# Optimization experiments

Measured on AMD Instinct MI355X. Metric: run time of the kernel, lower is better.

The kernel has to match this reference:

```python
import jax, jax.numpy as jnp
import numpy as np

N = 100000
E = 1600000
D_IN, D_HID, D_OUT = 128, 128, 64
SLOPE = 0.01


def setup_inputs() -> dict:
    key = jax.random.key(0)
    k1, k2, k3, k4 = jax.random.split(key, 4)
    x = jax.random.normal(k1, (N, D_IN), dtype=jnp.float32)
    edge_index = jax.random.randint(k2, (2, E), 0, N, dtype=jnp.int64)
    W1 = jax.random.normal(k3, (D_HID, D_IN), dtype=jnp.float32) * 0.05
    b1 = jnp.zeros((D_HID,), dtype=jnp.float32)
    W2 = jax.random.normal(k4, (D_OUT, D_HID), dtype=jnp.float32) * 0.05
    b2 = jnp.zeros((D_OUT,), dtype=jnp.float32)
    return {"x": x, "edge_index": edge_index, "W1": W1, "b1": b1, "W2": W2, "b2": b2}


def _gcn_norm(edge_index, num_nodes):
    # PyG GCNConv: add self loops, symmetric normalization deg^{-1/2} A_hat deg^{-1/2}
    loops = jnp.arange(num_nodes, dtype=edge_index.dtype)
    src = jnp.concatenate([edge_index[0], loops])
    dst = jnp.concatenate([edge_index[1], loops])
    deg = jax.ops.segment_sum(jnp.ones_like(dst, dtype=jnp.float32), dst, num_segments=num_nodes)
    dinv = jnp.where(deg > 0, jax.lax.rsqrt(deg), 0.0)
    norm = dinv[src] * dinv[dst]  # [E+N]
    return src, dst, norm


def _gcn_conv(x, src, dst, norm, W, b):
    h = x @ W.T                              # [N, out]
    msg = h[src] * norm[:, None]             # gather + edge scale: [E+N, out]
    agg = jax.ops.segment_sum(msg, dst, num_segments=x.shape[0])  # scatter-add
    return agg + b


def reference(x, edge_index, W1, b1, W2, b2):
    src, dst, norm = _gcn_norm(edge_index, x.shape[0])
    h1 = jax.nn.leaky_relu(_gcn_conv(x, src, dst, norm, W1, b1), negative_slope=SLOPE)
    h2 = _gcn_conv(h1, src, dst, norm, W2, b2)  # logits, no activation on last layer
    return (h1, h2)
```

## Files before the change

kernel.cpp:

```cpp
#include <hip/hip_runtime.h>


#define THREADS 256

typedef __attribute__((ext_vector_type(8))) short bf16x8;
typedef __attribute__((ext_vector_type(4))) float f32x4;

__device__ __forceinline__ short f2bf_rne(float f) {
    unsigned u = __builtin_bit_cast(unsigned, f);
    u = u + 0x7fffu + ((u >> 16) & 1u);
    return (short)(u >> 16);
}
__device__ __forceinline__ float bf2f(short h) {
    unsigned u = ((unsigned)(unsigned short)h) << 16;
    return __builtin_bit_cast(float, u);
}

__global__ __launch_bounds__(THREADS)
void count_kernel(const int* __restrict__ dst, int* __restrict__ counts, int E, int T) {
    int t = blockIdx.x * THREADS + threadIdx.x;
    int e0 = t, e1 = t + T, e2 = t + 2 * T, e3 = t + 3 * T;
    int d0 = dst[e0], d1 = dst[e1], d2 = dst[e2];
    bool v3 = e3 < E;
    int d3 = v3 ? dst[e3] : 0;
    atomicAdd(&counts[d0], 1);
    atomicAdd(&counts[d1], 1);
    atomicAdd(&counts[d2], 1);
    if (v3) atomicAdd(&counts[d3], 1);
}

__global__ __launch_bounds__(THREADS)
void scanA(const int* __restrict__ counts, int* __restrict__ rowptr,
           int* __restrict__ bsum, int n) {
    __shared__ int s[THREADS];
    int i = blockIdx.x * THREADS + threadIdx.x;
    int v = (i < n) ? counts[i] : 0;
    s[threadIdx.x] = v;
    __syncthreads();
    for (int off = 1; off < THREADS; off <<= 1) {
        int a = (threadIdx.x >= off) ? s[threadIdx.x - off] : 0;
        __syncthreads();
        s[threadIdx.x] += a;
        __syncthreads();
    }
    if (i < n) rowptr[i] = s[threadIdx.x] - v;
    if (threadIdx.x == THREADS - 1) bsum[blockIdx.x] = s[threadIdx.x];
}

__global__ __launch_bounds__(512)
void scanB(const int* __restrict__ bsum, int* __restrict__ boff, int nb) {
    __shared__ int s[512];
    int t = threadIdx.x;
    int v = (t < nb) ? bsum[t] : 0;
    s[t] = v;
    __syncthreads();
    for (int off = 1; off < 512; off <<= 1) {
        int a = (t >= off) ? s[t - off] : 0;
        __syncthreads();
        s[t] += a;
        __syncthreads();
    }
    if (t < nb) boff[t] = s[t] - v;
}

__global__ __launch_bounds__(THREADS)
void scanC(int* __restrict__ rowptr, int* __restrict__ cursor, float* __restrict__ dinv,
           const int* __restrict__ counts, const int* __restrict__ boff, int n) {
    int i = blockIdx.x * THREADS + threadIdx.x;
    if (i >= n) return;
    int r = rowptr[i] + boff[blockIdx.x];
    rowptr[i] = r;
    cursor[i] = r;
    dinv[i] = rsqrtf((float)counts[i] + 1.0f);
}

__global__ __launch_bounds__(THREADS)
void fill_kernel(const int* __restrict__ src, const int* __restrict__ dst,
                 int* __restrict__ cursor, int* __restrict__ csr, int E, int T) {
    int t = blockIdx.x * THREADS + threadIdx.x;
    int e0 = t, e1 = t + T, e2 = t + 2 * T, e3 = t + 3 * T;
    int d0 = dst[e0], d1 = dst[e1], d2 = dst[e2];
    int s0 = src[e0], s1 = src[e1], s2 = src[e2];
    bool v3 = e3 < E;
    int d3 = v3 ? dst[e3] : 0;
    int s3 = v3 ? src[e3] : 0;
    int p0 = atomicAdd(&cursor[d0], 1);
    int p1 = atomicAdd(&cursor[d1], 1);
    int p2 = atomicAdd(&cursor[d2], 1);
    int p3 = v3 ? atomicAdd(&cursor[d3], 1) : 0;
    csr[p0] = s0;
    csr[p1] = s1;
    csr[p2] = s2;
    if (v3) csr[p3] = s3;
}

template <int DO>
__global__ __launch_bounds__(THREADS)
void gemm_mfma(const float* __restrict__ X, const float* __restrict__ W,
               const float* __restrict__ dinv, float* __restrict__ G, int nrows) {
    constexpr int WCT = DO / 64;
    const int wid = threadIdx.x >> 6;
    const int lane = threadIdx.x & 63;
    const int l15 = lane & 15;
    const int lhi = lane >> 4;

    bf16x8 wh[WCT][4], wl[WCT][4];
#pragma unroll
    for (int ct = 0; ct < WCT; ct++) {
        const int j = (wid * WCT + ct) * 16 + l15;
#pragma unroll
        for (int kc = 0; kc < 4; kc++) {
            const float* wp = W + (size_t)j * 128 + kc * 32 + lhi * 8;
            float4 w0 = *(const float4*)wp;
            float4 w1 = *(const float4*)(wp + 4);
            float wv[8] = {w0.x, w0.y, w0.z, w0.w, w1.x, w1.y, w1.z, w1.w};
#pragma unroll
            for (int t = 0; t < 8; t++) {
                short h = f2bf_rne(wv[t]);
                wh[ct][kc][t] = h;
                wl[ct][kc][t] = f2bf_rne(wv[t] - bf2f(h));
            }
        }
    }

    for (int base = blockIdx.x * 16; base < nrows; base += gridDim.x * 16) {
        const int arow = base + l15;
        const bool av = arow < nrows;
        const float* xp = X + (size_t)arow * 128;
        bf16x8 ah[4], al[4];
#pragma unroll
        for (int kc = 0; kc < 4; kc++) {
            float4 a0 = make_float4(0.f, 0.f, 0.f, 0.f), a1 = a0;
            if (av) {
                a0 = *(const float4*)(xp + kc * 32 + lhi * 8);
                a1 = *(const float4*)(xp + kc * 32 + lhi * 8 + 4);
            }
            float xv[8] = {a0.x, a0.y, a0.z, a0.w, a1.x, a1.y, a1.z, a1.w};
#pragma unroll
            for (int t = 0; t < 8; t++) {
                short h = f2bf_rne(xv[t]);
                ah[kc][t] = h;
                al[kc][t] = f2bf_rne(xv[t] - bf2f(h));
            }
        }

        f32x4 acc[WCT];
#pragma unroll
        for (int ct = 0; ct < WCT; ct++) acc[ct] = (f32x4){0.f, 0.f, 0.f, 0.f};
#pragma unroll
        for (int kc = 0; kc < 4; kc++) {
#pragma unroll
            for (int ct = 0; ct < WCT; ct++) {
                acc[ct] = __builtin_amdgcn_mfma_f32_16x16x32_bf16(ah[kc], wh[ct][kc], acc[ct], 0, 0, 0);
                acc[ct] = __builtin_amdgcn_mfma_f32_16x16x32_bf16(ah[kc], wl[ct][kc], acc[ct], 0, 0, 0);
                acc[ct] = __builtin_amdgcn_mfma_f32_16x16x32_bf16(al[kc], wh[ct][kc], acc[ct], 0, 0, 0);
            }
        }

        float dv[4];
#pragma unroll
        for (int r = 0; r < 4; r++) {
            int row = base + lhi * 4 + r;
            dv[r] = (row < nrows) ? dinv[row] : 0.f;
        }
#pragma unroll
        for (int ct = 0; ct < WCT; ct++) {
            const int j = (wid * WCT + ct) * 16 + l15;
#pragma unroll
            for (int r = 0; r < 4; r++) {
                int row = base + lhi * 4 + r;
                if (row < nrows) G[(size_t)row * DO + j] = dv[r] * acc[ct][r];
            }
        }
    }
}

template <int DO, bool LEAKY>
__global__ __launch_bounds__(THREADS)
void aggregate(const int* __restrict__ rowptr, const int* __restrict__ counts,
               const int* __restrict__ csr, const float* __restrict__ g,
               const float* __restrict__ dinv, const float* __restrict__ bias,
               float* __restrict__ out, int n) {
    const int lane = threadIdx.x & 63;
    const int node = blockIdx.x * (THREADS / 64) + (threadIdx.x >> 6);
    if (node >= n) return;
    const int beg = rowptr[node], cnt = counts[node];

    if (DO == 128) {
        const int half = lane >> 5;
        const int hl = lane & 31;
        float4 a0 = make_float4(0.f, 0.f, 0.f, 0.f);
        float4 a1 = a0, a2 = a0, a3 = a0;
        for (int base = 0; base < cnt; base += 64) {
            int m = cnt - base; if (m > 64) m = 64;
            int sv = (base + lane < cnt) ? csr[beg + base + lane] : 0;
            int i = 0;
            for (; i + 8 <= m; i += 8) {
                int s0 = __shfl(sv, i + half);
                int s1 = __shfl(sv, i + 2 + half);
                int s2 = __shfl(sv, i + 4 + half);
                int s3 = __shfl(sv, i + 6 + half);
                float4 v0 = *(const float4*)(g + (size_t)s0 * 128 + hl * 4);
                float4 v1 = *(const float4*)(g + (size_t)s1 * 128 + hl * 4);
                float4 v2 = *(const float4*)(g + (size_t)s2 * 128 + hl * 4);
                float4 v3 = *(const float4*)(g + (size_t)s3 * 128 + hl * 4);
                a0.x += v0.x; a0.y += v0.y; a0.z += v0.z; a0.w += v0.w;
                a1.x += v1.x; a1.y += v1.y; a1.z += v1.z; a1.w += v1.w;
                a2.x += v2.x; a2.y += v2.y; a2.z += v2.z; a2.w += v2.w;
                a3.x += v3.x; a3.y += v3.y; a3.z += v3.z; a3.w += v3.w;
            }
            for (; i < m; i += 2) {
                int idx = i + half;
                int s = __shfl(sv, idx < m ? idx : 0);
                if (idx < m) {
                    float4 v = *(const float4*)(g + (size_t)s * 128 + hl * 4);
                    a0.x += v.x; a0.y += v.y; a0.z += v.z; a0.w += v.w;
                }
            }
        }
        a0.x += a1.x + a2.x + a3.x;
        a0.y += a1.y + a2.y + a3.y;
        a0.z += a1.z + a2.z + a3.z;
        a0.w += a1.w + a2.w + a3.w;
        a0.x += __shfl_xor(a0.x, 32);
        a0.y += __shfl_xor(a0.y, 32);
        a0.z += __shfl_xor(a0.z, 32);
        a0.w += __shfl_xor(a0.w, 32);
        if (half == 0) {
            float4 self = *(const float4*)(g + (size_t)node * 128 + hl * 4);
            float4 bv = ((const float4*)bias)[hl];
            float di = dinv[node];
            float4 r;
            r.x = di * (a0.x + self.x) + bv.x;
            r.y = di * (a0.y + self.y) + bv.y;
            r.z = di * (a0.z + self.z) + bv.z;
            r.w = di * (a0.w + self.w) + bv.w;
            if (LEAKY) {
                r.x = r.x > 0.f ? r.x : 0.01f * r.x;
                r.y = r.y > 0.f ? r.y : 0.01f * r.y;
                r.z = r.z > 0.f ? r.z : 0.01f * r.z;
                r.w = r.w > 0.f ? r.w : 0.01f * r.w;
            }
            *(float4*)(out + (size_t)node * 128 + hl * 4) = r;
        }
    } else {
        const int q = lane >> 4;
        const int ql = lane & 15;
        float4 a0 = make_float4(0.f, 0.f, 0.f, 0.f);
        float4 a1 = a0, a2 = a0, a3 = a0;
        for (int base = 0; base < cnt; base += 64) {
            int m = cnt - base; if (m > 64) m = 64;
            int sv = (base + lane < cnt) ? csr[beg + base + lane] : 0;
            int i = 0;
            for (; i + 16 <= m; i += 16) {
                int s0 = __shfl(sv, i + q);
                int s1 = __shfl(sv, i + 4 + q);
                int s2 = __shfl(sv, i + 8 + q);
                int s3 = __shfl(sv, i + 12 + q);
                float4 v0 = *(const float4*)(g + (size_t)s0 * 64 + ql * 4);
                float4 v1 = *(const float4*)(g + (size_t)s1 * 64 + ql * 4);
                float4 v2 = *(const float4*)(g + (size_t)s2 * 64 + ql * 4);
                float4 v3 = *(const float4*)(g + (size_t)s3 * 64 + ql * 4);
                a0.x += v0.x; a0.y += v0.y; a0.z += v0.z; a0.w += v0.w;
                a1.x += v1.x; a1.y += v1.y; a1.z += v1.z; a1.w += v1.w;
                a2.x += v2.x; a2.y += v2.y; a2.z += v2.z; a2.w += v2.w;
                a3.x += v3.x; a3.y += v3.y; a3.z += v3.z; a3.w += v3.w;
            }
            for (; i < m; i += 4) {
                int idx = i + q;
                int s = __shfl(sv, idx < m ? idx : 0);
                if (idx < m) {
                    float4 v = *(const float4*)(g + (size_t)s * 64 + ql * 4);
                    a0.x += v.x; a0.y += v.y; a0.z += v.z; a0.w += v.w;
                }
            }
        }
        a0.x += a1.x + a2.x + a3.x;
        a0.y += a1.y + a2.y + a3.y;
        a0.z += a1.z + a2.z + a3.z;
        a0.w += a1.w + a2.w + a3.w;
        a0.x += __shfl_xor(a0.x, 16); a0.x += __shfl_xor(a0.x, 32);
        a0.y += __shfl_xor(a0.y, 16); a0.y += __shfl_xor(a0.y, 32);
        a0.z += __shfl_xor(a0.z, 16); a0.z += __shfl_xor(a0.z, 32);
        a0.w += __shfl_xor(a0.w, 16); a0.w += __shfl_xor(a0.w, 32);
        if (q == 0) {
            float4 self = *(const float4*)(g + (size_t)node * 64 + ql * 4);
            float4 bv = ((const float4*)bias)[ql];
            float di = dinv[node];
            float4 r;
            r.x = di * (a0.x + self.x) + bv.x;
            r.y = di * (a0.y + self.y) + bv.y;
            r.z = di * (a0.z + self.z) + bv.z;
            r.w = di * (a0.w + self.w) + bv.w;
            if (LEAKY) {
                r.x = r.x > 0.f ? r.x : 0.01f * r.x;
                r.y = r.y > 0.f ? r.y : 0.01f * r.y;
                r.z = r.z > 0.f ? r.z : 0.01f * r.z;
                r.w = r.w > 0.f ? r.w : 0.01f * r.w;
            }
            *(float4*)(out + (size_t)node * 64 + ql * 4) = r;
        }
    }
}

extern "C" void kernel_launch(void* const* d_in, const int* in_sizes, int n_in,
                              void* d_out, int out_size, void* d_ws, size_t ws_size,
                              hipStream_t stream) {
    const float* x  = (const float*)d_in[0];
    const int*   ei = (const int*)d_in[1];
    const float* W1 = (const float*)d_in[2];
    const float* b1 = (const float*)d_in[3];
    const float* W2 = (const float*)d_in[4];
    const float* b2 = (const float*)d_in[5];

    const int N = in_sizes[0] / 128;
    const int E = in_sizes[1] / 2;
    const int* src = ei;
    const int* dst = ei + E;

    const int NB = (N + THREADS - 1) / THREADS;

    char* ws = (char*)d_ws;
    size_t off = 0;
    auto alloc = [&](size_t bytes) { char* p = ws + off; off = (off + bytes + 511) & ~(size_t)511; return p; };
    int*   counts = (int*)alloc((size_t)N * 4);
    int*   rowptr = (int*)alloc((size_t)N * 4);
    int*   cursor = (int*)alloc((size_t)N * 4);
    int*   bsum   = (int*)alloc((size_t)NB * 4);
    int*   boff   = (int*)alloc((size_t)NB * 4);
    float* dinv   = (float*)alloc((size_t)N * 4);
    int*   csr    = (int*)alloc((size_t)E * 4);
    float* g1     = (float*)alloc((size_t)N * 128 * 4);
    float* g2     = g1;

    float* h1 = (float*)d_out;
    float* h2 = h1 + (size_t)N * 128;

    hipMemsetAsync(counts, 0, (size_t)N * 4, stream);

    const int G4 = (E + 4 * THREADS - 1) / (4 * THREADS);
    const int T = G4 * THREADS;
    count_kernel<<<G4, THREADS, 0, stream>>>(dst, counts, E, T);
    scanA<<<NB, THREADS, 0, stream>>>(counts, rowptr, bsum, N);
    scanB<<<1, 512, 0, stream>>>(bsum, boff, NB);
    scanC<<<NB, THREADS, 0, stream>>>(rowptr, cursor, dinv, counts, boff, N);
    fill_kernel<<<G4, THREADS, 0, stream>>>(src, dst, cursor, csr, E, T);

    const int AGB = (N + (THREADS / 64) - 1) / (THREADS / 64);

    gemm_mfma<128><<<2048, THREADS, 0, stream>>>(x, W1, dinv, g1, N);
    aggregate<128, true><<<AGB, THREADS, 0, stream>>>(rowptr, counts, csr, g1, dinv, b1, h1, N);

    gemm_mfma<64><<<2048, THREADS, 0, stream>>>(h1, W2, dinv, g2, N);
    aggregate<64, false><<<AGB, THREADS, 0, stream>>>(rowptr, counts, csr, g2, dinv, b2, h2, N);
}
```

Baseline: 596.0 us.

## Fuse CSR fill with first GEMM and widen aggregation gather unrolling

Merges the CSR fill kernel and the layer-1 MFMA GEMM into one launch: even blocks do the fill and odd blocks do the GEMM, so the two independent phases run concurrently. The GEMM grid changes from 2048 blocks to G4 (about 1563). The aggregate kernels replace the 4-way unrolled gather plus remainder loop with a single masked 8-way unrolled loop that keeps 8 loads in flight. Risks include the GEMM blocks now pre-converting weights more often, more register pressure from 8 accumulators, and wasted masked iterations on low-degree nodes.

```diff
diff --git a/kernel.cpp b/kernel.cpp
--- a/kernel.cpp
+++ b/kernel.cpp
@@ -74,10 +74,10 @@
     dinv[i] = rsqrtf((float)counts[i] + 1.0f);
 }
 
-__global__ __launch_bounds__(THREADS)
-void fill_kernel(const int* __restrict__ src, const int* __restrict__ dst,
-                 int* __restrict__ cursor, int* __restrict__ csr, int E, int T) {
-    int t = blockIdx.x * THREADS + threadIdx.x;
+__device__ __forceinline__ void fill_body(int fbid, const int* __restrict__ src,
+                                          const int* __restrict__ dst, int* __restrict__ cursor,
+                                          int* __restrict__ csr, int E, int T) {
+    int t = fbid * THREADS + threadIdx.x;
     int e0 = t, e1 = t + T, e2 = t + 2 * T, e3 = t + 3 * T;
     int d0 = dst[e0], d1 = dst[e1], d2 = dst[e2];
     int s0 = src[e0], s1 = src[e1], s2 = src[e2];
@@ -95,9 +95,10 @@
 }
 
 template <int DO>
-__global__ __launch_bounds__(THREADS)
-void gemm_mfma(const float* __restrict__ X, const float* __restrict__ W,
-               const float* __restrict__ dinv, float* __restrict__ G, int nrows) {
+__device__ __forceinline__ void gemm_body(int gbid, int nGemm,
+                                          const float* __restrict__ X, const float* __restrict__ W,
+                                          const float* __restrict__ dinv, float* __restrict__ G,
+                                          int nrows) {
     constexpr int WCT = DO / 64;
     const int wid = threadIdx.x >> 6;
     const int lane = threadIdx.x & 63;
@@ -123,7 +124,7 @@
         }
     }
 
-    for (int base = blockIdx.x * 16; base < nrows; base += gridDim.x * 16) {
+    for (int base = gbid * 16; base < nrows; base += nGemm * 16) {
         const int arow = base + l15;
         const bool av = arow < nrows;
         const float* xp = X + (size_t)arow * 128;
@@ -173,6 +174,23 @@
             }
         }
     }
+}
+
+__global__ __launch_bounds__(THREADS)
+void fused_fill_gemm1(const int* __restrict__ src, const int* __restrict__ dst,
+                      int* __restrict__ cursor, int* __restrict__ csr, int E, int T,
+                      const float* __restrict__ X, const float* __restrict__ W,
+                      const float* __restrict__ dinv, float* __restrict__ G,
+                      int nrows, int nGemm) {
+    int bid = blockIdx.x;
+    if ((bid & 1) == 0) fill_body(bid >> 1, src, dst, cursor, csr, E, T);
+    else gemm_body<128>(bid >> 1, nGemm, X, W, dinv, G, nrows);
+}
+
+__global__ __launch_bounds__(THREADS)
+void gemm_mfma64(const float* __restrict__ X, const float* __restrict__ W,
+                 const float* __restrict__ dinv, float* __restrict__ G, int nrows) {
+    gemm_body<64>(blockIdx.x, gridDim.x, X, W, dinv, G, nrows);
 }
 
 template <int DO, bool LEAKY>
@@ -189,52 +207,41 @@
     if (DO == 128) {
         const int half = lane >> 5;
         const int hl = lane & 31;
-        float4 a0 = make_float4(0.f, 0.f, 0.f, 0.f);
-        float4 a1 = a0, a2 = a0, a3 = a0;
+        float4 a[8];
+#pragma unroll
+        for (int t = 0; t < 8; t++) a[t] = make_float4(0.f, 0.f, 0.f, 0.f);
         for (int base = 0; base < cnt; base += 64) {
             int m = cnt - base; if (m > 64) m = 64;
             int sv = (base + lane < cnt) ? csr[beg + base + lane] : 0;
-            int i = 0;
-            for (; i + 8 <= m; i += 8) {
-                int s0 = __shfl(sv, i + half);
-                int s1 = __shfl(sv, i + 2 + half);
-                int s2 = __shfl(sv, i + 4 + half);
-                int s3 = __shfl(sv, i + 6 + half);
-                float4 v0 = *(const float4*)(g + (size_t)s0 * 128 + hl * 4);
-                float4 v1 = *(const float4*)(g + (size_t)s1 * 128 + hl * 4);
-                float4 v2 = *(const float4*)(g + (size_t)s2 * 128 + hl * 4);
-                float4 v3 = *(const float4*)(g + (size_t)s3 * 128 + hl * 4);
-                a0.x += v0.x; a0.y += v0.y; a0.z += v0.z; a0.w += v0.w;
-                a1.x += v1.x; a1.y += v1.y; a1.z += v1.z; a1.w += v1.w;
-                a2.x += v2.x; a2.y += v2.y; a2.z += v2.z; a2.w += v2.w;
-                a3.x += v3.x; a3.y += v3.y; a3.z += v3.z; a3.w += v3.w;
-            }
-            for (; i < m; i += 2) {
-                int idx = i + half;
-                int s = __shfl(sv, idx < m ? idx : 0);
-                if (idx < m) {
-                    float4 v = *(const float4*)(g + (size_t)s * 128 + hl * 4);
-                    a0.x += v.x; a0.y += v.y; a0.z += v.z; a0.w += v.w;
+            for (int i = 0; i < m; i += 16) {
+#pragma unroll
+                for (int t = 0; t < 8; t++) {
+                    int idx = i + 2 * t + half;
+                    int s = __shfl(sv, idx & 63);
+                    if (idx < m) {
+                        float4 v = *(const float4*)(g + (size_t)s * 128 + hl * 4);
+                        a[t].x += v.x; a[t].y += v.y; a[t].z += v.z; a[t].w += v.w;
+                    }
                 }
             }
         }
-        a0.x += a1.x + a2.x + a3.x;
-        a0.y += a1.y + a2.y + a3.y;
-        a0.z += a1.z + a2.z + a3.z;
-        a0.w += a1.w + a2.w + a3.w;
-        a0.x += __shfl_xor(a0.x, 32);
-        a0.y += __shfl_xor(a0.y, 32);
-        a0.z += __shfl_xor(a0.z, 32);
-        a0.w += __shfl_xor(a0.w, 32);
+#pragma unroll
+        for (int t = 1; t < 8; t++) {
+            a[0].x += a[t].x; a[0].y += a[t].y; a[0].z += a[t].z; a[0].w += a[t].w;
+        }
+        a[0].x += __shfl_xor(a[0].x, 32);
+        a[0].y += __shfl_xor(a[0].y, 32);
+        a[0].z += __shfl_xor(a[0].z, 32);
+        a[0].w += __shfl_xor(a[0].w, 32);
         if (half == 0) {
             float4 self = *(const float4*)(g + (size_t)node * 128 + hl * 4);
             float4 bv = ((const float4*)bias)[hl];
             float di = dinv[node];
             float4 r;
-            r.x = di * (a0.x + self.x) + bv.x;
-            r.y = di * (a0.y + self.y) + bv.y;
-            r.z = di * (a0.z + self.z) + bv.z;
-            r.w = di * (a0.w + self.w) + bv.w;
+            r.x = di * (a[0].x + self.x) + bv.x;
+            r.y = di * (a[0].y + self.y) + bv.y;
+            r.z = di * (a[0].z + self.z) + bv.z;
+            r.w = di * (a[0].w + self.w) + bv.w;
             if (LEAKY) {
                 r.x = r.x > 0.f ? r.x : 0.01f * r.x;
                 r.y = r.y > 0.f ? r.y : 0.01f * r.y;
@@ -246,52 +253,41 @@
     } else {
         const int q = lane >> 4;
         const int ql = lane & 15;
-        float4 a0 = make_float4(0.f, 0.f, 0.f, 0.f);
-        float4 a1 = a0, a2 = a0, a3 = a0;
+        float4 a[8];
+#pragma unroll
+        for (int t = 0; t < 8; t++) a[t] = make_float4(0.f, 0.f, 0.f, 0.f);
         for (int base = 0; base < cnt; base += 64) {
             int m = cnt - base; if (m > 64) m = 64;
             int sv = (base + lane < cnt) ? csr[beg + base + lane] : 0;
-            int i = 0;
-            for (; i + 16 <= m; i += 16) {
-                int s0 = __shfl(sv, i + q);
-                int s1 = __shfl(sv, i + 4 + q);
-                int s2 = __shfl(sv, i + 8 + q);
-                int s3 = __shfl(sv, i + 12 + q);
-                float4 v0 = *(const float4*)(g + (size_t)s0 * 64 + ql * 4);
-                float4 v1 = *(const float4*)(g + (size_t)s1 * 64 + ql * 4);
-                float4 v2 = *(const float4*)(g + (size_t)s2 * 64 + ql * 4);
-                float4 v3 = *(const float4*)(g + (size_t)s3 * 64 + ql * 4);
-                a0.x += v0.x; a0.y += v0.y; a0.z += v0.z; a0.w += v0.w;
-                a1.x += v1.x; a1.y += v1.y; a1.z += v1.z; a1.w += v1.w;
-                a2.x += v2.x; a2.y += v2.y; a2.z += v2.z; a2.w += v2.w;
-                a3.x += v3.x; a3.y += v3.y; a3.z += v3.z; a3.w += v3.w;
-            }
-            for (; i < m; i += 4) {
-                int idx = i + q;
-                int s = __shfl(sv, idx < m ? idx : 0);
-                if (idx < m) {
-                    float4 v = *(const float4*)(g + (size_t)s * 64 + ql * 4);
-                    a0.x += v.x; a0.y += v.y; a0.z += v.z; a0.w += v.w;
+            for (int i = 0; i < m; i += 32) {
+#pragma unroll
+                for (int t = 0; t < 8; t++) {
+                    int idx = i + 4 * t + q;
+                    int s = __shfl(sv, idx & 63);
+                    if (idx < m) {
+                        float4 v = *(const float4*)(g + (size_t)s * 64 + ql * 4);
+                        a[t].x += v.x; a[t].y += v.y; a[t].z += v.z; a[t].w += v.w;
+                    }
                 }
             }
         }
-        a0.x += a1.x + a2.x + a3.x;
-        a0.y += a1.y + a2.y + a3.y;
-        a0.z += a1.z + a2.z + a3.z;
-        a0.w += a1.w + a2.w + a3.w;
-        a0.x += __shfl_xor(a0.x, 16); a0.x += __shfl_xor(a0.x, 32);
-        a0.y += __shfl_xor(a0.y, 16); a0.y += __shfl_xor(a0.y, 32);
-        a0.z += __shfl_xor(a0.z, 16); a0.z += __shfl_xor(a0.z, 32);
-        a0.w += __shfl_xor(a0.w, 16); a0.w += __shfl_xor(a0.w, 32);
+#pragma unroll
+        for (int t = 1; t < 8; t++) {
+            a[0].x += a[t].x; a[0].y += a[t].y; a[0].z += a[t].z; a[0].w += a[t].w;
+        }
+        a[0].x += __shfl_xor(a[0].x, 16); a[0].x += __shfl_xor(a[0].x, 32);
+        a[0].y += __shfl_xor(a[0].y, 16); a[0].y += __shfl_xor(a[0].y, 32);
+        a[0].z += __shfl_xor(a[0].z, 16); a[0].z += __shfl_xor(a[0].z, 32);
+        a[0].w += __shfl_xor(a[0].w, 16); a[0].w += __shfl_xor(a[0].w, 32);
         if (q == 0) {
             float4 self = *(const float4*)(g + (size_t)node * 64 + ql * 4);
             float4 bv = ((const float4*)bias)[ql];
             float di = dinv[node];
             float4 r;
-            r.x = di * (a0.x + self.x) + bv.x;
-            r.y = di * (a0.y + self.y) + bv.y;
-            r.z = di * (a0.z + self.z) + bv.z;
-            r.w = di * (a0.w + self.w) + bv.w;
+            r.x = di * (a[0].x + self.x) + bv.x;
+            r.y = di * (a[0].y + self.y) + bv.y;
+            r.z = di * (a[0].z + self.z) + bv.z;
+            r.w = di * (a[0].w + self.w) + bv.w;
             if (LEAKY) {
                 r.x = r.x > 0.f ? r.x : 0.01f * r.x;
                 r.y = r.y > 0.f ? r.y : 0.01f * r.y;
@@ -344,13 +340,13 @@
     scanA<<<NB, THREADS, 0, stream>>>(counts, rowptr, bsum, N);
     scanB<<<1, 512, 0, stream>>>(bsum, boff, NB);
     scanC<<<NB, THREADS, 0, stream>>>(rowptr, cursor, dinv, counts, boff, N);
-    fill_kernel<<<G4, THREADS, 0, stream>>>(src, dst, cursor, csr, E, T);
 
     const int AGB = (N + (THREADS / 64) - 1) / (THREADS / 64);
 
-    gemm_mfma<128><<<2048, THREADS, 0, stream>>>(x, W1, dinv, g1, N);
+    fused_fill_gemm1<<<2 * G4, THREADS, 0, stream>>>(src, dst, cursor, csr, E, T,
+                                                     x, W1, dinv, g1, N, G4);
     aggregate<128, true><<<AGB, THREADS, 0, stream>>>(rowptr, counts, csr, g1, dinv, b1, h1, N);
 
-    gemm_mfma<64><<<2048, THREADS, 0, stream>>>(h1, W2, dinv, g2, N);
+    gemm_mfma64<<<2048, THREADS, 0, stream>>>(h1, W2, dinv, g2, N);
     aggregate<64, false><<<AGB, THREADS, 0, stream>>>(rowptr, counts, csr, g2, dinv, b2, h2, N);
 }
```

Measured after the change: 557.4 us. 1.07x faster.
